# Performance work log

Measured on AMD Instinct MI355X. Metric: run time of the kernel, lower is better.

## Reference

```python
import jax, jax.numpy as jnp
import numpy as np

H = 1024   # hidden_size
I = 64     # input_window_size
OUT = 12   # fc output (hardcoded in module)

def _uniform(key, shape):
    return jax.random.uniform(key, shape, jnp.float32, -0.1, 0.1)

def setup_inputs() -> dict:
    key = jax.random.key(0)
    ks = jax.random.split(key, 9)
    x = jax.random.normal(ks[0], (256, 512, I), jnp.float32)
    # gate order i, f, g, o stacked along first axis -> [4H, in_dim]
    Wx0 = _uniform(ks[1], (4 * H, I))
    Wh0 = _uniform(ks[2], (4 * H, H))
    b0  = _uniform(ks[3], (4 * H,))
    Wx1 = _uniform(ks[4], (4 * H, H))
    Wh1 = _uniform(ks[5], (4 * H, H))
    b1  = _uniform(ks[6], (4 * H,))
    fc_W = _uniform(ks[7], (OUT, H))
    fc_b = _uniform(ks[8], (OUT,))
    return {"x": x, "Wx0": Wx0, "Wh0": Wh0, "b0": b0,
            "Wx1": Wx1, "Wh1": Wh1, "b1": b1,
            "fc_W": fc_W, "fc_b": fc_b}

def _cell(x_t, h_prev, c_prev, Wx, Wh, b):
    # fused gate GEMM: same math as 8 separate per-gate matmuls
    gates = x_t @ Wx.T + h_prev @ Wh.T + b  # [B, 4H]
    i_t = jax.nn.sigmoid(gates[:, 0 * H:1 * H])
    f_t = jax.nn.sigmoid(gates[:, 1 * H:2 * H])
    g_t = jnp.tanh(gates[:, 2 * H:3 * H])
    o_t = jax.nn.sigmoid(gates[:, 3 * H:4 * H])
    c_t = f_t * c_prev + i_t * g_t
    h_t = o_t * jnp.tanh(c_t)
    return h_t, c_t

def reference(x, Wx0, Wh0, b0, Wx1, Wh1, b1, fc_W, fc_b):
    B = x.shape[0]
    h0 = jnp.zeros((B, H), x.dtype)
    init = (h0, h0, h0, h0)  # (h_l0, c_l0, h_l1, c_l1)

    def step(carry, x_t):
        h0_, c0_, h1_, c1_ = carry
        h0n, c0n = _cell(x_t, h0_, c0_, Wx0, Wh0, b0)
        h1n, c1n = _cell(h0n, h1_, c1_, Wx1, Wh1, b1)
        return (h0n, c0n, h1n, c1n), None

    xs = jnp.swapaxes(x, 0, 1)  # [T, B, I]
    (h0f, c0f, h1f, c1f), _ = jax.lax.scan(step, init, xs)
    return h1f @ fc_W.T + fc_b  # [B, 12]
```

## Files before the change

### kernel.cpp

```cpp
#include <hip/hip_runtime.h>


typedef unsigned int u32;
typedef unsigned short u16;
typedef __attribute__((ext_vector_type(8))) short bf16x8;
typedef __attribute__((ext_vector_type(4))) float f32x4;

#define MFMA __builtin_amdgcn_mfma_f32_16x16x32_bf16
#define HB (256 * 1024)

__device__ __forceinline__ u16 f2bf(float f) {
  u32 u = __float_as_uint(f);
  u += 0x7fffu + ((u >> 16) & 1u);
  return (u16)(u >> 16);
}
__device__ __forceinline__ float sigm(float v) { return 1.f / (1.f + __expf(-v)); }
__device__ __forceinline__ float tanh_(float v) { return 1.f - 2.f / (__expf(2.f * v) + 1.f); }

__device__ __forceinline__ u32 ld_u32_sc01(const u32* p) {
  u32 v;
  asm volatile("global_load_dword %0, %1, off sc0 sc1\n\ts_waitcnt vmcnt(0)"
               : "=v"(v) : "v"(p) : "memory");
  return v;
}
__device__ __forceinline__ void st_u32_sc01(u32* p, u32 v) {
  asm volatile("global_store_dword %0, %1, off sc0 sc1" :: "v"(p), "v"(v) : "memory");
}
__device__ __forceinline__ void st_f32_sc01(float* p, float v) {
  asm volatile("global_store_dword %0, %1, off sc0 sc1" :: "v"(p), "v"(v) : "memory");
}

__global__ void __launch_bounds__(256) wconv(
    const float* __restrict__ Wx0, const float* __restrict__ Wh0,
    const float* __restrict__ Wx1, const float* __restrict__ Wh1,
    u16* __restrict__ W1p, u16* __restrict__ W0p, u16* __restrict__ X0p) {
  const u32 NG1 = 1048576u, NG0 = 524288u, NGX = 32768u;
  u32 g = blockIdx.x * 256u + threadIdx.x;
  const float* src; u16* dst;
  if (g < NG1) {
    u32 lane = g & 63u, f = (g >> 6) & 1u, jj = (g >> 7) & 1u, c = (g >> 8) & 7u;
    u32 kway = (g >> 11) & 3u, s = (g >> 13) & 1u, u0idx = g >> 14;
    u32 i15 = lane & 15u, kq = lane >> 4;
    u32 row = (2u * f + (i15 >> 3)) * 1024u + u0idx * 16u + s * 8u + (i15 & 7u);
    u32 k = (kway + 4u * (2u * c + jj)) * 32u + kq * 8u;
    src = (k < 1024u) ? Wx1 + (size_t)row * 1024 + k
                      : Wh1 + (size_t)row * 1024 + (k - 1024u);
    dst = W1p + (size_t)g * 8;
  } else if (g < NG1 + NG0) {
    u32 h = g - NG1;
    u32 lane = h & 63u, f = (h >> 6) & 1u, jj = (h >> 7) & 1u, c = (h >> 8) & 3u;
    u32 kway = (h >> 10) & 3u, s = (h >> 12) & 1u, u0idx = h >> 13;
    u32 i15 = lane & 15u, kq = lane >> 4;
    u32 row = (2u * f + (i15 >> 3)) * 1024u + u0idx * 16u + s * 8u + (i15 & 7u);
    u32 k = (kway + 4u * (2u * c + jj)) * 32u + kq * 8u;
    src = Wh0 + (size_t)row * 1024 + k;
    dst = W0p + (size_t)h * 8;
  } else if (g < NG1 + NG0 + NGX) {
    u32 h = g - NG1 - NG0;
    u32 lane = h & 63u, f = (h >> 6) & 1u, kway = (h >> 7) & 1u;
    u32 s = (h >> 8) & 1u, u0idx = h >> 9;
    u32 i15 = lane & 15u, kq = lane >> 4;
    u32 row = (2u * f + (i15 >> 3)) * 1024u + u0idx * 16u + s * 8u + (i15 & 7u);
    u32 k = kway * 32u + kq * 8u;
    src = Wx0 + (size_t)row * 64 + k;
    dst = X0p + (size_t)h * 8;
  } else return;
  float4 v0 = *(const float4*)src, v1 = *(const float4*)(src + 4);
  bf16x8 r;
  r[0] = (short)f2bf(v0.x); r[1] = (short)f2bf(v0.y);
  r[2] = (short)f2bf(v0.z); r[3] = (short)f2bf(v0.w);
  r[4] = (short)f2bf(v1.x); r[5] = (short)f2bf(v1.y);
  r[6] = (short)f2bf(v1.z); r[7] = (short)f2bf(v1.w);
  *(bf16x8*)dst = r;
}

#define LDW(bank, c) do {                                                      \
  u32 o0_ = bW[0] + (u32)((c) * 2048), o1_ = bW[1] + (u32)((c) * 2048);        \
  asm volatile("" : "+v"(o0_), "+v"(o1_));                                     \
  _Pragma("unroll")                                                            \
  for (int jj_ = 0; jj_ < 2; ++jj_)                                            \
    _Pragma("unroll")                                                          \
    for (int f_ = 0; f_ < 2; ++f_) {                                           \
      W[bank][jj_][0][f_] = *(const bf16x8*)(WP + o0_ + (u32)(jj_*1024+f_*512));\
      W[bank][jj_][1][f_] = *(const bf16x8*)(WP + o1_ + (u32)(jj_*1024+f_*512));\
    }                                                                          \
} while (0)

#define CHUNK(bank) do {                                                       \
  _Pragma("unroll")                                                            \
  for (int jj_ = 0; jj_ < 2; ++jj_) {                                          \
    const int kin_ = (kway + (jj_ << 2)) << 5;                                 \
    _Pragma("unroll")                                                          \
    for (int mf_ = 0; mf_ < 4; ++mf_) {                                        \
      bf16x8 a_ = readA(mf_, kin_);                                            \
      _Pragma("unroll")                                                        \
      for (int s_ = 0; s_ < 2; ++s_)                                           \
        _Pragma("unroll")                                                      \
        for (int f_ = 0; f_ < 2; ++f_)                                         \
          acc[mf_][s_][f_] = MFMA(a_, W[bank][jj_][s_][f_],                    \
                                  acc[mf_][s_][f_], 0, 0, 0);                  \
    }                                                                          \
  }                                                                            \
} while (0)

__global__ void __launch_bounds__(256, 2)
lstm_persist(const float* __restrict__ x,
             const float* __restrict__ b0, const float* __restrict__ b1,
             const float* __restrict__ fcW, const float* __restrict__ fcb,
             const u16* __restrict__ W1p, const u16* __restrict__ W0p,
             const u16* __restrict__ X0p,
             u16* __restrict__ h0b, u16* __restrict__ h1b,
             float* __restrict__ h1f, u32* __restrict__ bar,
             float* __restrict__ out)
{
  const int tid = threadIdx.x, blk = blockIdx.x;
  const int lane = tid & 63, w = tid >> 6;
  const int kway = w;
  const int L = blk >> 8;
  const int sub = blk & 255;
  const int m0 = (sub >> 6) << 6;
  const int u0idx = sub & 63;
  const int u0 = u0idx << 4;

  __shared__ short Abuf[64 * 256];
  __shared__ float gA[64][68];
  __shared__ float gB[64][68];
  __shared__ float cbuf[64][16];

  for (int i = tid; i < 64 * 16; i += 256) ((float*)cbuf)[i] = 0.f;

  const int i15 = lane & 15, kq = lane >> 4;

  u32 bW[2], bX[2];
#pragma unroll
  for (int s_ = 0; s_ < 2; ++s_) {
    u32 key = (u32)((u0idx << 1) | s_);
    bW[s_] = ((key << 2) | (u32)kway) * (L ? 16384u : 8192u) + (u32)lane * 8u;
    bX[s_] = ((key << 1) | (u32)kway) * 1024u + (u32)lane * 8u;
  }
  const u16* WP = L ? W1p : W0p;

  float bias[2][2];
#pragma unroll
  for (int s_ = 0; s_ < 2; ++s_)
#pragma unroll
    for (int f_ = 0; f_ < 2; ++f_) {
      int rowf = ((f_ << 1) + (i15 >> 3)) * 1024 + u0 + s_ * 8 + (i15 & 7);
      bias[s_][f_] = (kway == 0) ? (L ? b1[rowf] : b0[rowf]) : 0.f;
    }

  int grow[8], ldsoff[8];
#pragma unroll
  for (int cc = 0; cc < 8; ++cc) {
    int slot = cc * 256 + tid;
    int row = slot >> 5, c = slot & 31;
    grow[cc]   = ((m0 + row) << 10) + (c << 3);
    ldsoff[cc] = (row << 8) + ((c ^ (row & 7)) << 3);
  }

  bf16x8 v[8];
  auto stage_ld = [&](const u16* src, int kbase) {
#pragma unroll
    for (int cc = 0; cc < 8; ++cc)
      v[cc] = __builtin_nontemporal_load((const bf16x8*)(src + grow[cc] + kbase));
  };
  auto stage_st = [&]() {
#pragma unroll
    for (int cc = 0; cc < 8; ++cc)
      *(bf16x8*)&Abuf[ldsoff[cc]] = v[cc];
  };

  auto readA = [&](int mf, int kin) -> bf16x8 {
    int row = (mf << 4) | i15;
    int c = ((kin >> 3) + kq) ^ (row & 7);
    return *(const bf16x8*)&Abuf[(row << 8) + (c << 3)];
  };

  bf16x8 W[2][2][2][2];
  f32x4 acc[4][2][2];

  auto acc_init = [&]() {
#pragma unroll
    for (int mf = 0; mf < 4; ++mf)
#pragma unroll
      for (int s_ = 0; s_ < 2; ++s_)
#pragma unroll
        for (int f_ = 0; f_ < 2; ++f_) {
          float bv = bias[s_][f_];
          acc[mf][s_][f_][0] = bv; acc[mf][s_][f_][1] = bv;
          acc[mf][s_][f_][2] = bv; acc[mf][s_][f_][3] = bv;
        }
  };

  auto reduce2 = [&]() {
    if (kway < 2) {
      float (*g)[68] = kway ? gB : gA;
#pragma unroll
      for (int mf = 0; mf < 4; ++mf)
#pragma unroll
        for (int s_ = 0; s_ < 2; ++s_)
#pragma unroll
          for (int f_ = 0; f_ < 2; ++f_)
#pragma unroll
            for (int r = 0; r < 4; ++r)
              g[(mf << 4) + (kq << 2) + r][(s_ << 5) + (f_ << 4) + i15] = acc[mf][s_][f_][r];
    }
    __syncthreads();
    if (kway >= 2) {
      float (*g)[68] = (kway == 3) ? gB : gA;
#pragma unroll
      for (int mf = 0; mf < 4; ++mf)
#pragma unroll
        for (int s_ = 0; s_ < 2; ++s_)
#pragma unroll
          for (int f_ = 0; f_ < 2; ++f_)
#pragma unroll
            for (int r = 0; r < 4; ++r)
              g[(mf << 4) + (kq << 2) + r][(s_ << 5) + (f_ << 4) + i15] += acc[mf][s_][f_][r];
    }
    __syncthreads();
  };

  auto ew = [&](u16* hdst, bool wf32) {
    int row = tid >> 2, un = (tid & 3) << 2;
    float hq[4];
#pragma unroll
    for (int q = 0; q < 4; ++q) {
      int u = un + q;
      int cb = ((u >> 3) << 5) | (u & 7);
      float gi = gA[row][cb]      + gB[row][cb];
      float gf = gA[row][cb + 8]  + gB[row][cb + 8];
      float gg = gA[row][cb + 16] + gB[row][cb + 16];
      float go = gA[row][cb + 24] + gB[row][cb + 24];
      float ii = sigm(gi), ff = sigm(gf), g2 = tanh_(gg), oo = sigm(go);
      float c = ff * cbuf[row][u] + ii * g2;
      cbuf[row][u] = c;
      hq[q] = oo * tanh_(c);
    }
    size_t idx = ((size_t)(m0 + row) << 10) + u0 + un;
    st_u32_sc01((u32*)(hdst + idx),     (u32)f2bf(hq[0]) | ((u32)f2bf(hq[1]) << 16));
    st_u32_sc01((u32*)(hdst + idx + 2), (u32)f2bf(hq[2]) | ((u32)f2bf(hq[3]) << 16));
    if (wf32) {
      st_f32_sc01(h1f + idx,     hq[0]); st_f32_sc01(h1f + idx + 1, hq[1]);
      st_f32_sc01(h1f + idx + 2, hq[2]); st_f32_sc01(h1f + idx + 3, hq[3]);
    }
  };

  auto gridbar = [&](int t) {
    __syncthreads();
    if (tid == 0) {
      const int g = blk & 7;
      u32* gc   = bar + g * 32;
      u32* root = bar + 256;
      u32* gen  = bar + 288 + g * 32;
      const u32 p1 = (u32)(t + 1);
      __hip_atomic_fetch_add(gc, 1u, __ATOMIC_RELAXED, __HIP_MEMORY_SCOPE_AGENT);
      if (blk < 8) {
        while (ld_u32_sc01(gc) < 64u * p1) __builtin_amdgcn_s_sleep(4);
        __hip_atomic_fetch_add(root, 1u, __ATOMIC_RELAXED, __HIP_MEMORY_SCOPE_AGENT);
        while (ld_u32_sc01(root) < 8u * p1) __builtin_amdgcn_s_sleep(2);
        st_u32_sc01(gen, p1);
      } else {
        while (ld_u32_sc01(gen) < p1) __builtin_amdgcn_s_sleep(4);
      }
    }
    __syncthreads();
  };

  if (L == 0) {
    auto stage_x = [&](int t) {
      int row = tid >> 2, c4 = tid & 3;
      const float* g = x + ((size_t)(m0 + row) * 512 + t) * 64 + (c4 << 4);
      float4 a0 = *(const float4*)g,       a1 = *(const float4*)(g + 4);
      float4 a2 = *(const float4*)(g + 8), a3 = *(const float4*)(g + 12);
      bf16x8 r0, r1;
      r0[0] = (short)f2bf(a0.x); r0[1] = (short)f2bf(a0.y);
      r0[2] = (short)f2bf(a0.z); r0[3] = (short)f2bf(a0.w);
      r0[4] = (short)f2bf(a1.x); r0[5] = (short)f2bf(a1.y);
      r0[6] = (short)f2bf(a1.z); r0[7] = (short)f2bf(a1.w);
      r1[0] = (short)f2bf(a2.x); r1[1] = (short)f2bf(a2.y);
      r1[2] = (short)f2bf(a2.z); r1[3] = (short)f2bf(a2.w);
      r1[4] = (short)f2bf(a3.x); r1[5] = (short)f2bf(a3.y);
      r1[6] = (short)f2bf(a3.z); r1[7] = (short)f2bf(a3.w);
      int c = c4 << 1;
      *(bf16x8*)&Abuf[(row << 8) + (((c    ) ^ (row & 7)) << 3)] = r0;
      *(bf16x8*)&Abuf[(row << 8) + (((c + 1) ^ (row & 7)) << 3)] = r1;
    };

#pragma unroll 1
    for (int t = 0; t <= 512; ++t) {
      if (t < 512) {
        const u16* h0rd = h0b + ((t + 1) & 1) * HB;
        u16* h0wr = h0b + (t & 1) * HB;
        acc_init();
        stage_x(t);
        stage_ld(h0rd, 0);
        bf16x8 X[2][2];
        if (kway < 2) {
          u32 ox0 = bX[0], ox1 = bX[1];
          asm volatile("" : "+v"(ox0), "+v"(ox1));
          X[0][0] = *(const bf16x8*)(X0p + ox0);
          X[0][1] = *(const bf16x8*)(X0p + ox0 + 512u);
          X[1][0] = *(const bf16x8*)(X0p + ox1);
          X[1][1] = *(const bf16x8*)(X0p + ox1 + 512u);
        }
        LDW(0, 0);
        __syncthreads();
        if (kway < 2) {
          const int kin = kway << 5;
#pragma unroll
          for (int mf = 0; mf < 4; ++mf) {
            bf16x8 a = readA(mf, kin);
#pragma unroll
            for (int s_ = 0; s_ < 2; ++s_)
#pragma unroll
              for (int f_ = 0; f_ < 2; ++f_)
                acc[mf][s_][f_] = MFMA(a, X[s_][f_], acc[mf][s_][f_], 0, 0, 0);
          }
        }
        __syncthreads();
        stage_st(); __syncthreads();
        stage_ld(h0rd, 256); LDW(1, 1); CHUNK(0); __syncthreads();
        stage_st(); __syncthreads();
        stage_ld(h0rd, 512); LDW(0, 2); CHUNK(1); __syncthreads();
        stage_st(); __syncthreads();
        stage_ld(h0rd, 768); LDW(1, 3); CHUNK(0); __syncthreads();
        stage_st(); __syncthreads();
        CHUNK(1);
        reduce2();
        ew(h0wr, false);
      }
      gridbar(t);
    }
  } else {
#pragma unroll 1
    for (int t = 0; t <= 512; ++t) {
      if (t >= 1) {
        const u16* h0rd = h0b + ((t + 1) & 1) * HB;
        const u16* h1rd = h1b + (t & 1) * HB;
        u16* h1wr = h1b + ((t + 1) & 1) * HB;
        acc_init();
        stage_ld(h0rd, 0); LDW(0, 0);
        stage_st(); __syncthreads();
        stage_ld(h0rd, 256); LDW(1, 1); CHUNK(0); __syncthreads();
        stage_st(); __syncthreads();
        stage_ld(h0rd, 512); LDW(0, 2); CHUNK(1); __syncthreads();
        stage_st(); __syncthreads();
        stage_ld(h0rd, 768); LDW(1, 3); CHUNK(0); __syncthreads();
        stage_st(); __syncthreads();
        stage_ld(h1rd, 0);   LDW(0, 4); CHUNK(1); __syncthreads();
        stage_st(); __syncthreads();
        stage_ld(h1rd, 256); LDW(1, 5); CHUNK(0); __syncthreads();
        stage_st(); __syncthreads();
        stage_ld(h1rd, 512); LDW(0, 6); CHUNK(1); __syncthreads();
        stage_st(); __syncthreads();
        stage_ld(h1rd, 768); LDW(1, 7); CHUNK(0); __syncthreads();
        stage_st(); __syncthreads();
        CHUNK(1);
        reduce2();
        ew(h1wr, t == 512);
      }
      gridbar(t);
    }
  }

  if (blk < 64) {
    const int row = (blk << 2) | w;
    const float* hrow = h1f + ((size_t)row << 10);
#pragma unroll 1
    for (int o = 0; o < 12; ++o) {
      const float* wrow = fcW + o * 1024;
      float p = 0.f;
#pragma unroll
      for (int j = 0; j < 16; ++j) {
        int k = (j << 6) | lane;
        p += __builtin_nontemporal_load(hrow + k) * wrow[k];
      }
#pragma unroll
      for (int off = 32; off > 0; off >>= 1) p += __shfl_down(p, off, 64);
      if (lane == 0) out[row * 12 + o] = p + fcb[o];
    }
  }
}

extern "C" void kernel_launch(void* const* d_in, const int* in_sizes, int n_in,
                              void* d_out, int out_size, void* d_ws, size_t ws_size,
                              hipStream_t stream) {
  (void)in_sizes; (void)n_in; (void)out_size; (void)ws_size;
  const float* x   = (const float*)d_in[0];
  const float* Wx0 = (const float*)d_in[1];
  const float* Wh0 = (const float*)d_in[2];
  const float* b0  = (const float*)d_in[3];
  const float* Wx1 = (const float*)d_in[4];
  const float* Wh1 = (const float*)d_in[5];
  const float* b1  = (const float*)d_in[6];
  const float* fcW = (const float*)d_in[7];
  const float* fcb = (const float*)d_in[8];

  char* ws = (char*)d_ws;
  u16* W1p   = (u16*)ws;
  u16* W0p   = (u16*)(ws + (16u << 20));
  u16* X0p   = (u16*)(ws + (24u << 20));
  u16* h0b   = (u16*)(ws + (25u << 20));
  u16* h1b   = (u16*)(ws + (26u << 20));
  float* h1f = (float*)(ws + (27u << 20));
  u32* bar   = (u32*)(ws + (28u << 20));

  hipMemsetAsync(ws + (25u << 20) + (1 << 19), 0, 1 << 19, stream);
  hipMemsetAsync(ws + (26u << 20) + (1 << 19), 0, 1 << 19, stream);
  hipMemsetAsync(bar, 0, 4096, stream);

  wconv<<<6272, 256, 0, stream>>>(Wx0, Wh0, Wx1, Wh1, W1p, W0p, X0p);
  lstm_persist<<<512, 256, 0, stream>>>(x, b0, b1, fcW, fcb,
                                        W1p, W0p, X0p,
                                        h0b, h1b, h1f, bar, (float*)d_out);
}
```

Measured before the change: 8.451 ms.

## Give each wave a private LDS slice for its K-slice and drop per-chunk block barriers

Each wave now stages only the hidden-state columns it consumes (its own kway slice) into a wave-private LDS region. This removes the __syncthreads between every stage and compute step inside a timestep, and the x-input staging is folded into the same per-wave layout. The grid barrier is also flattened: one wave polls all eight group counters with shuffles, replacing the two-level tree. The cost is fewer threads sharing each load, W reloads no longer double-buffered across banks, and more global atomic polling traffic.

```diff
diff --git a/kernel.cpp b/kernel.cpp
--- a/kernel.cpp
+++ b/kernel.cpp
@@ -74,31 +74,29 @@
   *(bf16x8*)dst = r;
 }
 
-#define LDW(bank, c) do {                                                      \
-  u32 o0_ = bW[0] + (u32)((c) * 2048), o1_ = bW[1] + (u32)((c) * 2048);        \
+#define LDW(c) do {                                                            \
+  u32 o0_ = bW0 + (u32)((c) * 2048), o1_ = bW1 + (u32)((c) * 2048);            \
   asm volatile("" : "+v"(o0_), "+v"(o1_));                                     \
   _Pragma("unroll")                                                            \
   for (int jj_ = 0; jj_ < 2; ++jj_)                                            \
     _Pragma("unroll")                                                          \
     for (int f_ = 0; f_ < 2; ++f_) {                                           \
-      W[bank][jj_][0][f_] = *(const bf16x8*)(WP + o0_ + (u32)(jj_*1024+f_*512));\
-      W[bank][jj_][1][f_] = *(const bf16x8*)(WP + o1_ + (u32)(jj_*1024+f_*512));\
+      W[jj_][0][f_] = *(const bf16x8*)(WP + o0_ + (u32)(jj_*1024 + f_*512));   \
+      W[jj_][1][f_] = *(const bf16x8*)(WP + o1_ + (u32)(jj_*1024 + f_*512));   \
     }                                                                          \
 } while (0)
 
-#define CHUNK(bank) do {                                                       \
+#define CHUNK() do {                                                           \
   _Pragma("unroll")                                                            \
   for (int jj_ = 0; jj_ < 2; ++jj_) {                                          \
-    const int kin_ = (kway + (jj_ << 2)) << 5;                                 \
     _Pragma("unroll")                                                          \
     for (int mf_ = 0; mf_ < 4; ++mf_) {                                        \
-      bf16x8 a_ = readA(mf_, kin_);                                            \
+      bf16x8 a_ = readA(mf_, jj_);                                             \
       _Pragma("unroll")                                                        \
       for (int s_ = 0; s_ < 2; ++s_)                                           \
         _Pragma("unroll")                                                      \
         for (int f_ = 0; f_ < 2; ++f_)                                         \
-          acc[mf_][s_][f_] = MFMA(a_, W[bank][jj_][s_][f_],                    \
-                                  acc[mf_][s_][f_], 0, 0, 0);                  \
+          acc[mf_][s_][f_] = MFMA(a_, W[jj_][s_][f_], acc[mf_][s_][f_], 0,0,0);\
     }                                                                          \
   }                                                                            \
 } while (0)
@@ -122,7 +120,7 @@
   const int u0idx = sub & 63;
   const int u0 = u0idx << 4;
 
-  __shared__ short Abuf[64 * 256];
+  __shared__ short Awv[4][4096];
   __shared__ float gA[64][68];
   __shared__ float gB[64][68];
   __shared__ float cbuf[64][16];
@@ -131,13 +129,11 @@
 
   const int i15 = lane & 15, kq = lane >> 4;
 
-  u32 bW[2], bX[2];
-#pragma unroll
-  for (int s_ = 0; s_ < 2; ++s_) {
-    u32 key = (u32)((u0idx << 1) | s_);
-    bW[s_] = ((key << 2) | (u32)kway) * (L ? 16384u : 8192u) + (u32)lane * 8u;
-    bX[s_] = ((key << 1) | (u32)kway) * 1024u + (u32)lane * 8u;
-  }
+  const u32 key0 = (u32)((u0idx << 1) | 0), key1 = (u32)((u0idx << 1) | 1);
+  const u32 bW0 = ((key0 << 2) | (u32)kway) * (L ? 16384u : 8192u) + (u32)lane * 8u;
+  const u32 bW1 = ((key1 << 2) | (u32)kway) * (L ? 16384u : 8192u) + (u32)lane * 8u;
+  const u32 bX0 = ((key0 << 1) | (u32)kway) * 1024u + (u32)lane * 8u;
+  const u32 bX1 = ((key1 << 1) | (u32)kway) * 1024u + (u32)lane * 8u;
   const u16* WP = L ? W1p : W0p;
 
   float bias[2][2];
@@ -149,34 +145,35 @@
       bias[s_][f_] = (kway == 0) ? (L ? b1[rowf] : b0[rowf]) : 0.f;
     }
 
-  int grow[8], ldsoff[8];
+  int goff[8], lds16[8];
 #pragma unroll
   for (int cc = 0; cc < 8; ++cc) {
-    int slot = cc * 256 + tid;
-    int row = slot >> 5, c = slot & 31;
-    grow[cc]   = ((m0 + row) << 10) + (c << 3);
-    ldsoff[cc] = (row << 8) + ((c ^ (row & 7)) << 3);
+    int sid = cc * 64 + lane;
+    int row = sid >> 3, jj = (sid >> 2) & 1, kq4 = sid & 3;
+    goff[cc]  = ((m0 + row) << 10) + jj * 128 + kq4 * 8;
+    lds16[cc] = row * 64 + (((((jj << 2) | kq4) ^ (row & 7))) << 3);
   }
 
   bf16x8 v[8];
-  auto stage_ld = [&](const u16* src, int kbase) {
+  auto ld_h = [&](const u16* src, int cm) {
+    const int colb = (kway << 5) + (cm << 8);
 #pragma unroll
     for (int cc = 0; cc < 8; ++cc)
-      v[cc] = __builtin_nontemporal_load((const bf16x8*)(src + grow[cc] + kbase));
-  };
-  auto stage_st = [&]() {
+      v[cc] = __builtin_nontemporal_load((const bf16x8*)(src + goff[cc] + colb));
+  };
+  auto dsw = [&]() {
 #pragma unroll
     for (int cc = 0; cc < 8; ++cc)
-      *(bf16x8*)&Abuf[ldsoff[cc]] = v[cc];
-  };
-
-  auto readA = [&](int mf, int kin) -> bf16x8 {
+      *(bf16x8*)&Awv[kway][lds16[cc]] = v[cc];
+  };
+
+  auto readA = [&](int mf, int jj) -> bf16x8 {
     int row = (mf << 4) | i15;
-    int c = ((kin >> 3) + kq) ^ (row & 7);
-    return *(const bf16x8*)&Abuf[(row << 8) + (c << 3)];
-  };
-
-  bf16x8 W[2][2][2][2];
+    int sl = ((jj << 2) | kq) ^ (row & 7);
+    return *(const bf16x8*)&Awv[kway][row * 64 + (sl << 3)];
+  };
+
+  bf16x8 W[2][2][2];
   f32x4 acc[4][2][2];
 
   auto acc_init = [&]() {
@@ -248,115 +245,92 @@
 
   auto gridbar = [&](int t) {
     __syncthreads();
-    if (tid == 0) {
-      const int g = blk & 7;
-      u32* gc   = bar + g * 32;
-      u32* root = bar + 256;
-      u32* gen  = bar + 288 + g * 32;
+    if (w == 0) {
       const u32 p1 = (u32)(t + 1);
-      __hip_atomic_fetch_add(gc, 1u, __ATOMIC_RELAXED, __HIP_MEMORY_SCOPE_AGENT);
-      if (blk < 8) {
-        while (ld_u32_sc01(gc) < 64u * p1) __builtin_amdgcn_s_sleep(4);
-        __hip_atomic_fetch_add(root, 1u, __ATOMIC_RELAXED, __HIP_MEMORY_SCOPE_AGENT);
-        while (ld_u32_sc01(root) < 8u * p1) __builtin_amdgcn_s_sleep(2);
-        st_u32_sc01(gen, p1);
-      } else {
-        while (ld_u32_sc01(gen) < p1) __builtin_amdgcn_s_sleep(4);
+      if (lane == 0)
+        __hip_atomic_fetch_add(bar + (blk & 7) * 32, 1u,
+                               __ATOMIC_RELAXED, __HIP_MEMORY_SCOPE_AGENT);
+      const u32 target = 512u * p1;
+      for (;;) {
+        u32 vv = 0;
+        if (lane < 8) vv = ld_u32_sc01(bar + lane * 32);
+        vv += __shfl_xor(vv, 1); vv += __shfl_xor(vv, 2); vv += __shfl_xor(vv, 4);
+        if (__shfl(vv, 0) >= target) break;
+        __builtin_amdgcn_s_sleep(1);
       }
     }
     __syncthreads();
   };
 
-  if (L == 0) {
-    auto stage_x = [&](int t) {
-      int row = tid >> 2, c4 = tid & 3;
-      const float* g = x + ((size_t)(m0 + row) * 512 + t) * 64 + (c4 << 4);
-      float4 a0 = *(const float4*)g,       a1 = *(const float4*)(g + 4);
-      float4 a2 = *(const float4*)(g + 8), a3 = *(const float4*)(g + 12);
-      bf16x8 r0, r1;
-      r0[0] = (short)f2bf(a0.x); r0[1] = (short)f2bf(a0.y);
-      r0[2] = (short)f2bf(a0.z); r0[3] = (short)f2bf(a0.w);
-      r0[4] = (short)f2bf(a1.x); r0[5] = (short)f2bf(a1.y);
-      r0[6] = (short)f2bf(a1.z); r0[7] = (short)f2bf(a1.w);
-      r1[0] = (short)f2bf(a2.x); r1[1] = (short)f2bf(a2.y);
-      r1[2] = (short)f2bf(a2.z); r1[3] = (short)f2bf(a2.w);
-      r1[4] = (short)f2bf(a3.x); r1[5] = (short)f2bf(a3.y);
-      r1[6] = (short)f2bf(a3.z); r1[7] = (short)f2bf(a3.w);
-      int c = c4 << 1;
-      *(bf16x8*)&Abuf[(row << 8) + (((c    ) ^ (row & 7)) << 3)] = r0;
-      *(bf16x8*)&Abuf[(row << 8) + (((c + 1) ^ (row & 7)) << 3)] = r1;
-    };
+  int gxoff[4], ldsx[4];
+#pragma unroll
+  for (int cc = 0; cc < 4; ++cc) {
+    int sid = cc * 64 + lane;
+    int row = sid >> 2, kq4 = sid & 3;
+    gxoff[cc] = (m0 + row) * 32768 + kway * 32 + kq4 * 8;
+    ldsx[cc]  = row * 64 + ((kq4 ^ (row & 7)) << 3);
+  }
 
 #pragma unroll 1
-    for (int t = 0; t <= 512; ++t) {
+  for (int t = 0; t <= 512; ++t) {
+    if (L == 0) {
       if (t < 512) {
         const u16* h0rd = h0b + ((t + 1) & 1) * HB;
         u16* h0wr = h0b + (t & 1) * HB;
         acc_init();
-        stage_x(t);
-        stage_ld(h0rd, 0);
-        bf16x8 X[2][2];
+        ld_h(h0rd, 0);
         if (kway < 2) {
-          u32 ox0 = bX[0], ox1 = bX[1];
+#pragma unroll
+          for (int cc = 0; cc < 4; ++cc) {
+            const float* g = x + gxoff[cc] + t * 64;
+            float4 a0 = *(const float4*)g, a1 = *(const float4*)(g + 4);
+            bf16x8 r;
+            r[0] = (short)f2bf(a0.x); r[1] = (short)f2bf(a0.y);
+            r[2] = (short)f2bf(a0.z); r[3] = (short)f2bf(a0.w);
+            r[4] = (short)f2bf(a1.x); r[5] = (short)f2bf(a1.y);
+            r[6] = (short)f2bf(a1.z); r[7] = (short)f2bf(a1.w);
+            *(bf16x8*)&Awv[kway][ldsx[cc]] = r;
+          }
+          u32 ox0 = bX0, ox1 = bX1;
           asm volatile("" : "+v"(ox0), "+v"(ox1));
-          X[0][0] = *(const bf16x8*)(X0p + ox0);
-          X[0][1] = *(const bf16x8*)(X0p + ox0 + 512u);
-          X[1][0] = *(const bf16x8*)(X0p + ox1);
-          X[1][1] = *(const bf16x8*)(X0p + ox1 + 512u);
-        }
-        LDW(0, 0);
-        __syncthreads();
-        if (kway < 2) {
-          const int kin = kway << 5;
+          bf16x8 X00 = *(const bf16x8*)(X0p + ox0);
+          bf16x8 X01 = *(const bf16x8*)(X0p + ox0 + 512u);
+          bf16x8 X10 = *(const bf16x8*)(X0p + ox1);
+          bf16x8 X11 = *(const bf16x8*)(X0p + ox1 + 512u);
 #pragma unroll
           for (int mf = 0; mf < 4; ++mf) {
-            bf16x8 a = readA(mf, kin);
-#pragma unroll
-            for (int s_ = 0; s_ < 2; ++s_)
-#pragma unroll
-              for (int f_ = 0; f_ < 2; ++f_)
-                acc[mf][s_][f_] = MFMA(a, X[s_][f_], acc[mf][s_][f_], 0, 0, 0);
+            int row = (mf << 4) | i15;
+            bf16x8 a = *(const bf16x8*)&Awv[kway][row * 64 + ((kq ^ (row & 7)) << 3)];
+            acc[mf][0][0] = MFMA(a, X00, acc[mf][0][0], 0, 0, 0);
+            acc[mf][0][1] = MFMA(a, X01, acc[mf][0][1], 0, 0, 0);
+            acc[mf][1][0] = MFMA(a, X10, acc[mf][1][0], 0, 0, 0);
+            acc[mf][1][1] = MFMA(a, X11, acc[mf][1][1], 0, 0, 0);
           }
         }
-        __syncthreads();
-        stage_st(); __syncthreads();
-        stage_ld(h0rd, 256); LDW(1, 1); CHUNK(0); __syncthreads();
-        stage_st(); __syncthreads();
-        stage_ld(h0rd, 512); LDW(0, 2); CHUNK(1); __syncthreads();
-        stage_st(); __syncthreads();
-        stage_ld(h0rd, 768); LDW(1, 3); CHUNK(0); __syncthreads();
-        stage_st(); __syncthreads();
-        CHUNK(1);
+        dsw();
+        ld_h(h0rd, 1); LDW(0); CHUNK(); dsw();
+        ld_h(h0rd, 2); LDW(1); CHUNK(); dsw();
+        ld_h(h0rd, 3); LDW(2); CHUNK(); dsw();
+        LDW(3); CHUNK();
         reduce2();
         ew(h0wr, false);
       }
       gridbar(t);
-    }
-  } else {
-#pragma unroll 1
-    for (int t = 0; t <= 512; ++t) {
+    } else {
       if (t >= 1) {
         const u16* h0rd = h0b + ((t + 1) & 1) * HB;
         const u16* h1rd = h1b + (t & 1) * HB;
         u16* h1wr = h1b + ((t + 1) & 1) * HB;
         acc_init();
-        stage_ld(h0rd, 0); LDW(0, 0);
-        stage_st(); __syncthreads();
-        stage_ld(h0rd, 256); LDW(1, 1); CHUNK(0); __syncthreads();
-        stage_st(); __syncthreads();
-        stage_ld(h0rd, 512); LDW(0, 2); CHUNK(1); __syncthreads();
-        stage_st(); __syncthreads();
-        stage_ld(h0rd, 768); LDW(1, 3); CHUNK(0); __syncthreads();
-        stage_st(); __syncthreads();
-        stage_ld(h1rd, 0);   LDW(0, 4); CHUNK(1); __syncthreads();
-        stage_st(); __syncthreads();
-        stage_ld(h1rd, 256); LDW(1, 5); CHUNK(0); __syncthreads();
-        stage_st(); __syncthreads();
-        stage_ld(h1rd, 512); LDW(0, 6); CHUNK(1); __syncthreads();
-        stage_st(); __syncthreads();
-        stage_ld(h1rd, 768); LDW(1, 7); CHUNK(0); __syncthreads();
-        stage_st(); __syncthreads();
-        CHUNK(1);
+        ld_h(h0rd, 0); dsw();
+        ld_h(h0rd, 1); LDW(0); CHUNK(); dsw();
+        ld_h(h0rd, 2); LDW(1); CHUNK(); dsw();
+        ld_h(h0rd, 3); LDW(2); CHUNK(); dsw();
+        ld_h(h1rd, 0); LDW(3); CHUNK(); dsw();
+        ld_h(h1rd, 1); LDW(4); CHUNK(); dsw();
+        ld_h(h1rd, 2); LDW(5); CHUNK(); dsw();
+        ld_h(h1rd, 3); LDW(6); CHUNK(); dsw();
+        LDW(7); CHUNK();
         reduce2();
         ew(h1wr, t == 512);
       }
```

Measured after the change: 17.63 ms. 2.09x slower.

## Double-buffer LDS A tiles to halve barriers per chunk in LSTM loop

Applied to the files above, without the earlier changes.

Replaces the single LDS A buffer with two buffers placed in a union with the gate-reduction scratch. Each chunk stores the next staged tile into the alternate buffer while MFMAs read the current one, so each chunk needs one __syncthreads instead of two. Shared memory use stays the same because the reduction buffers are aliased onto the A buffers. The two layer loops are also merged into a single time loop that branches on the layer. This costs an extra barrier before the reduction, and the aliased memory must not be overwritten while still in use.

```diff
diff --git a/kernel.cpp b/kernel.cpp
--- a/kernel.cpp
+++ b/kernel.cpp
@@ -86,13 +86,13 @@
     }                                                                          \
 } while (0)
 
-#define CHUNK(bank) do {                                                       \
+#define CHUNK(bsel, bank) do {                                                 \
   _Pragma("unroll")                                                            \
   for (int jj_ = 0; jj_ < 2; ++jj_) {                                          \
     const int kin_ = (kway + (jj_ << 2)) << 5;                                 \
     _Pragma("unroll")                                                          \
     for (int mf_ = 0; mf_ < 4; ++mf_) {                                        \
-      bf16x8 a_ = readA(mf_, kin_);                                            \
+      bf16x8 a_ = readA(bsel, mf_, kin_);                                      \
       _Pragma("unroll")                                                        \
       for (int s_ = 0; s_ < 2; ++s_)                                           \
         _Pragma("unroll")                                                      \
@@ -102,6 +102,11 @@
     }                                                                          \
   }                                                                            \
 } while (0)
+
+union SMemU {
+  short Ab[2][16384];
+  float G[2][64][68];
+};
 
 __global__ void __launch_bounds__(256, 2)
 lstm_persist(const float* __restrict__ x,
@@ -122,9 +127,7 @@
   const int u0idx = sub & 63;
   const int u0 = u0idx << 4;
 
-  __shared__ short Abuf[64 * 256];
-  __shared__ float gA[64][68];
-  __shared__ float gB[64][68];
+  __shared__ SMemU sm;
   __shared__ float cbuf[64][16];
 
   for (int i = tid; i < 64 * 16; i += 256) ((float*)cbuf)[i] = 0.f;
@@ -164,16 +167,16 @@
     for (int cc = 0; cc < 8; ++cc)
       v[cc] = __builtin_nontemporal_load((const bf16x8*)(src + grow[cc] + kbase));
   };
-  auto stage_st = [&]() {
+  auto stage_st = [&](int bsel) {
 #pragma unroll
     for (int cc = 0; cc < 8; ++cc)
-      *(bf16x8*)&Abuf[ldsoff[cc]] = v[cc];
-  };
-
-  auto readA = [&](int mf, int kin) -> bf16x8 {
+      *(bf16x8*)&sm.Ab[bsel][ldsoff[cc]] = v[cc];
+  };
+
+  auto readA = [&](int bsel, int mf, int kin) -> bf16x8 {
     int row = (mf << 4) | i15;
     int c = ((kin >> 3) + kq) ^ (row & 7);
-    return *(const bf16x8*)&Abuf[(row << 8) + (c << 3)];
+    return *(const bf16x8*)&sm.Ab[bsel][(row << 8) + (c << 3)];
   };
 
   bf16x8 W[2][2][2][2];
@@ -194,7 +197,7 @@
 
   auto reduce2 = [&]() {
     if (kway < 2) {
-      float (*g)[68] = kway ? gB : gA;
+      float (*g)[68] = sm.G[kway];
 #pragma unroll
       for (int mf = 0; mf < 4; ++mf)
 #pragma unroll
@@ -207,7 +210,7 @@
     }
     __syncthreads();
     if (kway >= 2) {
-      float (*g)[68] = (kway == 3) ? gB : gA;
+      float (*g)[68] = sm.G[kway - 2];
 #pragma unroll
       for (int mf = 0; mf < 4; ++mf)
 #pragma unroll
@@ -228,10 +231,10 @@
     for (int q = 0; q < 4; ++q) {
       int u = un + q;
       int cb = ((u >> 3) << 5) | (u & 7);
-      float gi = gA[row][cb]      + gB[row][cb];
-      float gf = gA[row][cb + 8]  + gB[row][cb + 8];
-      float gg = gA[row][cb + 16] + gB[row][cb + 16];
-      float go = gA[row][cb + 24] + gB[row][cb + 24];
+      float gi = sm.G[0][row][cb]      + sm.G[1][row][cb];
+      float gf = sm.G[0][row][cb + 8]  + sm.G[1][row][cb + 8];
+      float gg = sm.G[0][row][cb + 16] + sm.G[1][row][cb + 16];
+      float go = sm.G[0][row][cb + 24] + sm.G[1][row][cb + 24];
       float ii = sigm(gi), ff = sigm(gf), g2 = tanh_(gg), oo = sigm(go);
       float c = ff * cbuf[row][u] + ii * g2;
       cbuf[row][u] = c;
@@ -267,34 +270,33 @@
     __syncthreads();
   };
 
-  if (L == 0) {
-    auto stage_x = [&](int t) {
-      int row = tid >> 2, c4 = tid & 3;
-      const float* g = x + ((size_t)(m0 + row) * 512 + t) * 64 + (c4 << 4);
-      float4 a0 = *(const float4*)g,       a1 = *(const float4*)(g + 4);
-      float4 a2 = *(const float4*)(g + 8), a3 = *(const float4*)(g + 12);
-      bf16x8 r0, r1;
-      r0[0] = (short)f2bf(a0.x); r0[1] = (short)f2bf(a0.y);
-      r0[2] = (short)f2bf(a0.z); r0[3] = (short)f2bf(a0.w);
-      r0[4] = (short)f2bf(a1.x); r0[5] = (short)f2bf(a1.y);
-      r0[6] = (short)f2bf(a1.z); r0[7] = (short)f2bf(a1.w);
-      r1[0] = (short)f2bf(a2.x); r1[1] = (short)f2bf(a2.y);
-      r1[2] = (short)f2bf(a2.z); r1[3] = (short)f2bf(a2.w);
-      r1[4] = (short)f2bf(a3.x); r1[5] = (short)f2bf(a3.y);
-      r1[6] = (short)f2bf(a3.z); r1[7] = (short)f2bf(a3.w);
-      int c = c4 << 1;
-      *(bf16x8*)&Abuf[(row << 8) + (((c    ) ^ (row & 7)) << 3)] = r0;
-      *(bf16x8*)&Abuf[(row << 8) + (((c + 1) ^ (row & 7)) << 3)] = r1;
-    };
-
 #pragma unroll 1
-    for (int t = 0; t <= 512; ++t) {
+  for (int t = 0; t <= 512; ++t) {
+    if (L == 0) {
       if (t < 512) {
         const u16* h0rd = h0b + ((t + 1) & 1) * HB;
         u16* h0wr = h0b + (t & 1) * HB;
         acc_init();
-        stage_x(t);
+        {
+          int row = tid >> 2, c4 = tid & 3;
+          const float* g = x + ((size_t)(m0 + row) * 512 + t) * 64 + (c4 << 4);
+          float4 a0 = *(const float4*)g,       a1 = *(const float4*)(g + 4);
+          float4 a2 = *(const float4*)(g + 8), a3 = *(const float4*)(g + 12);
+          bf16x8 r0, r1;
+          r0[0] = (short)f2bf(a0.x); r0[1] = (short)f2bf(a0.y);
+          r0[2] = (short)f2bf(a0.z); r0[3] = (short)f2bf(a0.w);
+          r0[4] = (short)f2bf(a1.x); r0[5] = (short)f2bf(a1.y);
+          r0[6] = (short)f2bf(a1.z); r0[7] = (short)f2bf(a1.w);
+          r1[0] = (short)f2bf(a2.x); r1[1] = (short)f2bf(a2.y);
+          r1[2] = (short)f2bf(a2.z); r1[3] = (short)f2bf(a2.w);
+          r1[4] = (short)f2bf(a3.x); r1[5] = (short)f2bf(a3.y);
+          r1[6] = (short)f2bf(a3.z); r1[7] = (short)f2bf(a3.w);
+          int c = c4 << 1;
+          *(bf16x8*)&sm.Ab[0][(row << 8) + (((c    ) ^ (row & 7)) << 3)] = r0;
+          *(bf16x8*)&sm.Ab[0][(row << 8) + (((c + 1) ^ (row & 7)) << 3)] = r1;
+        }
         stage_ld(h0rd, 0);
+        LDW(0, 0);
         bf16x8 X[2][2];
         if (kway < 2) {
           u32 ox0 = bX[0], ox1 = bX[1];
@@ -304,13 +306,12 @@
           X[1][0] = *(const bf16x8*)(X0p + ox1);
           X[1][1] = *(const bf16x8*)(X0p + ox1 + 512u);
         }
-        LDW(0, 0);
         __syncthreads();
         if (kway < 2) {
           const int kin = kway << 5;
 #pragma unroll
           for (int mf = 0; mf < 4; ++mf) {
-            bf16x8 a = readA(mf, kin);
+            bf16x8 a = readA(0, mf, kin);
 #pragma unroll
             for (int s_ = 0; s_ < 2; ++s_)
 #pragma unroll
@@ -318,45 +319,34 @@
                 acc[mf][s_][f_] = MFMA(a, X[s_][f_], acc[mf][s_][f_], 0, 0, 0);
           }
         }
+        stage_st(1);
         __syncthreads();
-        stage_st(); __syncthreads();
-        stage_ld(h0rd, 256); LDW(1, 1); CHUNK(0); __syncthreads();
-        stage_st(); __syncthreads();
-        stage_ld(h0rd, 512); LDW(0, 2); CHUNK(1); __syncthreads();
-        stage_st(); __syncthreads();
-        stage_ld(h0rd, 768); LDW(1, 3); CHUNK(0); __syncthreads();
-        stage_st(); __syncthreads();
-        CHUNK(1);
+        stage_ld(h0rd, 256); LDW(1, 1); CHUNK(1, 0); stage_st(0); __syncthreads();
+        stage_ld(h0rd, 512); LDW(0, 2); CHUNK(0, 1); stage_st(1); __syncthreads();
+        stage_ld(h0rd, 768); LDW(1, 3); CHUNK(1, 0); stage_st(0); __syncthreads();
+        CHUNK(0, 1);
+        __syncthreads();
         reduce2();
         ew(h0wr, false);
       }
       gridbar(t);
-    }
-  } else {
-#pragma unroll 1
-    for (int t = 0; t <= 512; ++t) {
+    } else {
       if (t >= 1) {
         const u16* h0rd = h0b + ((t + 1) & 1) * HB;
         const u16* h1rd = h1b + (t & 1) * HB;
         u16* h1wr = h1b + ((t + 1) & 1) * HB;
         acc_init();
         stage_ld(h0rd, 0); LDW(0, 0);
-        stage_st(); __syncthreads();
-        stage_ld(h0rd, 256); LDW(1, 1); CHUNK(0); __syncthreads();
-        stage_st(); __syncthreads();
-        stage_ld(h0rd, 512); LDW(0, 2); CHUNK(1); __syncthreads();
-        stage_st(); __syncthreads();
-        stage_ld(h0rd, 768); LDW(1, 3); CHUNK(0); __syncthreads();
-        stage_st(); __syncthreads();
-        stage_ld(h1rd, 0);   LDW(0, 4); CHUNK(1); __syncthreads();
-        stage_st(); __syncthreads();
-        stage_ld(h1rd, 256); LDW(1, 5); CHUNK(0); __syncthreads();
-        stage_st(); __syncthreads();
-        stage_ld(h1rd, 512); LDW(0, 6); CHUNK(1); __syncthreads();
-        stage_st(); __syncthreads();
-        stage_ld(h1rd, 768); LDW(1, 7); CHUNK(0); __syncthreads();
-        stage_st(); __syncthreads();
-        CHUNK(1);
+        stage_st(0); __syncthreads();
+        stage_ld(h0rd, 256); LDW(1, 1); CHUNK(0, 0); stage_st(1); __syncthreads();
+        stage_ld(h0rd, 512); LDW(0, 2); CHUNK(1, 1); stage_st(0); __syncthreads();
+        stage_ld(h0rd, 768); LDW(1, 3); CHUNK(0, 0); stage_st(1); __syncthreads();
+        stage_ld(h1rd, 0);   LDW(0, 4); CHUNK(1, 1); stage_st(0); __syncthreads();
+        stage_ld(h1rd, 256); LDW(1, 5); CHUNK(0, 0); stage_st(1); __syncthreads();
+        stage_ld(h1rd, 512); LDW(0, 6); CHUNK(1, 1); stage_st(0); __syncthreads();
+        stage_ld(h1rd, 768); LDW(1, 7); CHUNK(0, 0); stage_st(1); __syncthreads();
+        CHUNK(1, 1);
+        __syncthreads();
         reduce2();
         ew(h1wr, t == 512);
       }
```

Result: slower. 10.63 ms (+25.8%).

## Load MFMA A-operands directly from global into registers, dropping LDS staging

Applied to the files above, without the earlier changes.

The hidden-state A fragments are now loaded straight from global memory into per-wave register banks in MFMA layout, replacing the cooperative global→LDS staging with swizzle and the many __syncthreads per chunk. The x input for layer 0 is likewise loaded and converted per-wave directly into registers. Scheduling barriers separate the double-buffered stages. This removes LDS traffic and block-wide barriers but makes each wave issue its own narrower, less coalesced global loads, with rows duplicated across waves, and raises register pressure.

```diff
diff --git a/kernel.cpp b/kernel.cpp
--- a/kernel.cpp
+++ b/kernel.cpp
@@ -8,6 +8,7 @@
 
 #define MFMA __builtin_amdgcn_mfma_f32_16x16x32_bf16
 #define HB (256 * 1024)
+#define SCHED0 __builtin_amdgcn_sched_barrier(0)
 
 __device__ __forceinline__ u16 f2bf(float f) {
   u32 u = __float_as_uint(f);
@@ -86,13 +87,24 @@
     }                                                                          \
 } while (0)
 
+#define LDA(bank, srcp, cb) do {                                               \
+  u32 ob_ = (u32)(cb);                                                         \
+  asm volatile("" : "+v"(ob_));                                                \
+  const char* p_ = (const char*)(srcp);                                        \
+  _Pragma("unroll")                                                            \
+  for (int jj_ = 0; jj_ < 2; ++jj_)                                            \
+    _Pragma("unroll")                                                          \
+    for (int mf_ = 0; mf_ < 4; ++mf_)                                          \
+      Ab[bank][jj_][mf_] = __builtin_nontemporal_load(                         \
+        (const bf16x8*)(p_ + aoffb[mf_] + ob_ + (u32)(jj_ * 256)));            \
+} while (0)
+
 #define CHUNK(bank) do {                                                       \
   _Pragma("unroll")                                                            \
-  for (int jj_ = 0; jj_ < 2; ++jj_) {                                          \
-    const int kin_ = (kway + (jj_ << 2)) << 5;                                 \
+  for (int jj_ = 0; jj_ < 2; ++jj_)                                            \
     _Pragma("unroll")                                                          \
     for (int mf_ = 0; mf_ < 4; ++mf_) {                                        \
-      bf16x8 a_ = readA(mf_, kin_);                                            \
+      bf16x8 a_ = Ab[bank][jj_][mf_];                                          \
       _Pragma("unroll")                                                        \
       for (int s_ = 0; s_ < 2; ++s_)                                           \
         _Pragma("unroll")                                                      \
@@ -100,7 +112,6 @@
           acc[mf_][s_][f_] = MFMA(a_, W[bank][jj_][s_][f_],                    \
                                   acc[mf_][s_][f_], 0, 0, 0);                  \
     }                                                                          \
-  }                                                                            \
 } while (0)
 
 __global__ void __launch_bounds__(256, 2)
@@ -122,7 +133,6 @@
   const int u0idx = sub & 63;
   const int u0 = u0idx << 4;
 
-  __shared__ short Abuf[64 * 256];
   __shared__ float gA[64][68];
   __shared__ float gB[64][68];
   __shared__ float cbuf[64][16];
@@ -149,33 +159,12 @@
       bias[s_][f_] = (kway == 0) ? (L ? b1[rowf] : b0[rowf]) : 0.f;
     }
 
-  int grow[8], ldsoff[8];
-#pragma unroll
-  for (int cc = 0; cc < 8; ++cc) {
-    int slot = cc * 256 + tid;
-    int row = slot >> 5, c = slot & 31;
-    grow[cc]   = ((m0 + row) << 10) + (c << 3);
-    ldsoff[cc] = (row << 8) + ((c ^ (row & 7)) << 3);
-  }
-
-  bf16x8 v[8];
-  auto stage_ld = [&](const u16* src, int kbase) {
-#pragma unroll
-    for (int cc = 0; cc < 8; ++cc)
-      v[cc] = __builtin_nontemporal_load((const bf16x8*)(src + grow[cc] + kbase));
-  };
-  auto stage_st = [&]() {
-#pragma unroll
-    for (int cc = 0; cc < 8; ++cc)
-      *(bf16x8*)&Abuf[ldsoff[cc]] = v[cc];
-  };
-
-  auto readA = [&](int mf, int kin) -> bf16x8 {
-    int row = (mf << 4) | i15;
-    int c = ((kin >> 3) + kq) ^ (row & 7);
-    return *(const bf16x8*)&Abuf[(row << 8) + (c << 3)];
-  };
-
+  u32 aoffb[4];
+#pragma unroll
+  for (int mf = 0; mf < 4; ++mf)
+    aoffb[mf] = (u32)(((((m0 + (mf << 4) + i15) << 10) + (kway << 5) + (kq << 3)) << 1));
+
+  bf16x8 Ab[2][2][4];
   bf16x8 W[2][2][2][2];
   f32x4 acc[4][2][2];
 
@@ -268,64 +257,46 @@
   };
 
   if (L == 0) {
-    auto stage_x = [&](int t) {
-      int row = tid >> 2, c4 = tid & 3;
-      const float* g = x + ((size_t)(m0 + row) * 512 + t) * 64 + (c4 << 4);
-      float4 a0 = *(const float4*)g,       a1 = *(const float4*)(g + 4);
-      float4 a2 = *(const float4*)(g + 8), a3 = *(const float4*)(g + 12);
-      bf16x8 r0, r1;
-      r0[0] = (short)f2bf(a0.x); r0[1] = (short)f2bf(a0.y);
-      r0[2] = (short)f2bf(a0.z); r0[3] = (short)f2bf(a0.w);
-      r0[4] = (short)f2bf(a1.x); r0[5] = (short)f2bf(a1.y);
-      r0[6] = (short)f2bf(a1.z); r0[7] = (short)f2bf(a1.w);
-      r1[0] = (short)f2bf(a2.x); r1[1] = (short)f2bf(a2.y);
-      r1[2] = (short)f2bf(a2.z); r1[3] = (short)f2bf(a2.w);
-      r1[4] = (short)f2bf(a3.x); r1[5] = (short)f2bf(a3.y);
-      r1[6] = (short)f2bf(a3.z); r1[7] = (short)f2bf(a3.w);
-      int c = c4 << 1;
-      *(bf16x8*)&Abuf[(row << 8) + (((c    ) ^ (row & 7)) << 3)] = r0;
-      *(bf16x8*)&Abuf[(row << 8) + (((c + 1) ^ (row & 7)) << 3)] = r1;
-    };
-
 #pragma unroll 1
     for (int t = 0; t <= 512; ++t) {
       if (t < 512) {
         const u16* h0rd = h0b + ((t + 1) & 1) * HB;
         u16* h0wr = h0b + (t & 1) * HB;
         acc_init();
-        stage_x(t);
-        stage_ld(h0rd, 0);
-        bf16x8 X[2][2];
+        LDA(0, h0rd, 0); LDW(0, 0);
         if (kway < 2) {
+          const char* xt = (const char*)x + (size_t)m0 * 131072u + (size_t)t * 256u;
+          const u32 oxw = (u32)(((kway << 5) + (kq << 3)) << 2);
+          bf16x8 ax[4];
+#pragma unroll
+          for (int mf = 0; mf < 4; ++mf) {
+            const float* g = (const float*)(xt + (size_t)((mf << 4) + i15) * 131072u + oxw);
+            float4 a0 = *(const float4*)g, a1 = *(const float4*)(g + 4);
+            bf16x8 r;
+            r[0] = (short)f2bf(a0.x); r[1] = (short)f2bf(a0.y);
+            r[2] = (short)f2bf(a0.z); r[3] = (short)f2bf(a0.w);
+            r[4] = (short)f2bf(a1.x); r[5] = (short)f2bf(a1.y);
+            r[6] = (short)f2bf(a1.z); r[7] = (short)f2bf(a1.w);
+            ax[mf] = r;
+          }
           u32 ox0 = bX[0], ox1 = bX[1];
           asm volatile("" : "+v"(ox0), "+v"(ox1));
-          X[0][0] = *(const bf16x8*)(X0p + ox0);
-          X[0][1] = *(const bf16x8*)(X0p + ox0 + 512u);
-          X[1][0] = *(const bf16x8*)(X0p + ox1);
-          X[1][1] = *(const bf16x8*)(X0p + ox1 + 512u);
-        }
-        LDW(0, 0);
-        __syncthreads();
-        if (kway < 2) {
-          const int kin = kway << 5;
+          bf16x8 X00 = *(const bf16x8*)(X0p + ox0);
+          bf16x8 X01 = *(const bf16x8*)(X0p + ox0 + 512u);
+          bf16x8 X10 = *(const bf16x8*)(X0p + ox1);
+          bf16x8 X11 = *(const bf16x8*)(X0p + ox1 + 512u);
 #pragma unroll
           for (int mf = 0; mf < 4; ++mf) {
-            bf16x8 a = readA(mf, kin);
-#pragma unroll
-            for (int s_ = 0; s_ < 2; ++s_)
-#pragma unroll
-              for (int f_ = 0; f_ < 2; ++f_)
-                acc[mf][s_][f_] = MFMA(a, X[s_][f_], acc[mf][s_][f_], 0, 0, 0);
+            acc[mf][0][0] = MFMA(ax[mf], X00, acc[mf][0][0], 0, 0, 0);
+            acc[mf][0][1] = MFMA(ax[mf], X01, acc[mf][0][1], 0, 0, 0);
+            acc[mf][1][0] = MFMA(ax[mf], X10, acc[mf][1][0], 0, 0, 0);
+            acc[mf][1][1] = MFMA(ax[mf], X11, acc[mf][1][1], 0, 0, 0);
           }
         }
-        __syncthreads();
-        stage_st(); __syncthreads();
-        stage_ld(h0rd, 256); LDW(1, 1); CHUNK(0); __syncthreads();
-        stage_st(); __syncthreads();
-        stage_ld(h0rd, 512); LDW(0, 2); CHUNK(1); __syncthreads();
-        stage_st(); __syncthreads();
-        stage_ld(h0rd, 768); LDW(1, 3); CHUNK(0); __syncthreads();
-        stage_st(); __syncthreads();
+        SCHED0;
+        LDA(1, h0rd, 512);  LDW(1, 1); CHUNK(0); SCHED0;
+        LDA(0, h0rd, 1024); LDW(0, 2); CHUNK(1); SCHED0;
+        LDA(1, h0rd, 1536); LDW(1, 3); CHUNK(0); SCHED0;
         CHUNK(1);
         reduce2();
         ew(h0wr, false);
@@ -340,22 +311,14 @@
         const u16* h1rd = h1b + (t & 1) * HB;
         u16* h1wr = h1b + ((t + 1) & 1) * HB;
         acc_init();
-        stage_ld(h0rd, 0); LDW(0, 0);
-        stage_st(); __syncthreads();
-        stage_ld(h0rd, 256); LDW(1, 1); CHUNK(0); __syncthreads();
-        stage_st(); __syncthreads();
-        stage_ld(h0rd, 512); LDW(0, 2); CHUNK(1); __syncthreads();
-        stage_st(); __syncthreads();
-        stage_ld(h0rd, 768); LDW(1, 3); CHUNK(0); __syncthreads();
-        stage_st(); __syncthreads();
-        stage_ld(h1rd, 0);   LDW(0, 4); CHUNK(1); __syncthreads();
-        stage_st(); __syncthreads();
-        stage_ld(h1rd, 256); LDW(1, 5); CHUNK(0); __syncthreads();
-        stage_st(); __syncthreads();
-        stage_ld(h1rd, 512); LDW(0, 6); CHUNK(1); __syncthreads();
-        stage_st(); __syncthreads();
-        stage_ld(h1rd, 768); LDW(1, 7); CHUNK(0); __syncthreads();
-        stage_st(); __syncthreads();
+        LDA(0, h0rd, 0);    LDW(0, 0); SCHED0;
+        LDA(1, h0rd, 512);  LDW(1, 1); CHUNK(0); SCHED0;
+        LDA(0, h0rd, 1024); LDW(0, 2); CHUNK(1); SCHED0;
+        LDA(1, h0rd, 1536); LDW(1, 3); CHUNK(0); SCHED0;
+        LDA(0, h1rd, 0);    LDW(0, 4); CHUNK(1); SCHED0;
+        LDA(1, h1rd, 512);  LDW(1, 5); CHUNK(0); SCHED0;
+        LDA(0, h1rd, 1024); LDW(0, 6); CHUNK(1); SCHED0;
+        LDA(1, h1rd, 1536); LDW(1, 7); CHUNK(0); SCHED0;
         CHUNK(1);
         reduce2();
         ew(h1wr, t == 512);
```

Result: slower. 12.34 ms (+46.1%).
